# Optimization experiments

Hardware: AMD Instinct MI355X
Metric: run time of the kernel (lower is better)

## Reference

```python
import jax, jax.numpy as jnp
import numpy as np

B, C, H, W = 256, 3, 256, 256
ROT_DEG = 180.0
COLOR = 0.3
CROP = 256


def _sample_bilinear(img, ix, iy, zeros_pad):
    # img: [B,C,H,W]; ix, iy: [B,Ho,Wo] pixel-space coords
    Hh, Ww = img.shape[2], img.shape[3]
    x0 = jnp.floor(ix)
    y0 = jnp.floor(iy)
    wx = ix - x0
    wy = iy - y0

    def gather(yy, xx):
        yc = jnp.clip(yy, 0, Hh - 1).astype(jnp.int32)
        xc = jnp.clip(xx, 0, Ww - 1).astype(jnp.int32)
        v = jax.vmap(lambda im, y, x: im[:, y, x])(img, yc, xc)  # [B,C,Ho,Wo]
        if zeros_pad:  # torch grid_sample padding_mode='zeros': zero each OOB corner
            valid = ((yy >= 0) & (yy <= Hh - 1) & (xx >= 0) & (xx <= Ww - 1))
            v = v * valid[:, None].astype(img.dtype)
        return v

    return (gather(y0, x0) * ((1 - wy) * (1 - wx))[:, None]
            + gather(y0, x0 + 1) * ((1 - wy) * wx)[:, None]
            + gather(y0 + 1, x0) * (wy * (1 - wx))[:, None]
            + gather(y0 + 1, x0 + 1) * (wy * wx)[:, None])


def setup_inputs() -> dict:
    key = jax.random.key(0)
    ks = jax.random.split(key, 8)
    return {
        'images': jax.random.normal(ks[0], (B, C, H, W), dtype=jnp.float32),
        'rand_theta': jax.random.uniform(ks[1], (B,), dtype=jnp.float32),
        'rand_flip': jax.random.uniform(ks[2], (B,), dtype=jnp.float32),
        'rand_sizes': jax.random.uniform(ks[3], (B, 2), dtype=jnp.float32),
        'rand_shifts': jax.random.uniform(ks[4], (B, 2), dtype=jnp.float32),
        'rand_delta': jax.random.uniform(ks[5], (B, 1, 1, 1), dtype=jnp.float32),
        'rand_mag1': jax.random.uniform(ks[6], (B, 1, 1, 1), dtype=jnp.float32),
        'rand_mag2': jax.random.uniform(ks[7], (B, 1, 1, 1), dtype=jnp.float32),
    }


def reference(images, rand_theta, rand_flip, rand_sizes, rand_shifts,
              rand_delta, rand_mag1, rand_mag2):
    b, c, h, w = images.shape
    dt = images.dtype

    # ---- per-sample rotation: affine_grid + grid_sample (align_corners=False, zeros pad)
    theta = (rand_theta * 2 - 1) * (ROT_DEG * np.pi / 180.0)
    cth, sth = jnp.cos(theta), jnp.sin(theta)  # G_inv = rotate2d(theta)
    xn = (2 * jnp.arange(w, dtype=dt) + 1) / w - 1  # [W] normalized coords
    yn = (2 * jnp.arange(h, dtype=dt) + 1) / h - 1  # [H]
    xg = xn[None, None, :]
    yg = yn[None, :, None]
    xp = cth[:, None, None] * xg - sth[:, None, None] * yg  # [B,H,W]
    yp = sth[:, None, None] * xg + cth[:, None, None] * yg
    ix = ((xp + 1) * w - 1) / 2
    iy = ((yp + 1) * h - 1) / 2
    images = _sample_bilinear(images, ix, iy, zeros_pad=True)

    # ---- random horizontal flip
    flip = rand_flip > 0.5
    images = jnp.where(flip[:, None, None, None], images[..., ::-1], images)

    # ---- per-sample zoom (bilinear resize, align_corners=True) + shifted center crop
    sizes = jnp.round(h * (rand_sizes / 4 + 1.0) - 0.5)  # [B,2], values in [256, 320]
    max_shifts = sizes - CROP
    shift_ranges = max_shifts - 1e-5
    shifts = jnp.round(rand_shifts * shift_ranges - shift_ranges / 2)
    start = jnp.floor(max_shifts / 2) + shifts  # crop start (sh, sw), [B,2]
    ys = jnp.arange(h, dtype=dt)
    xs = jnp.arange(w, dtype=dt)
    # crop pixel (y,x) in the resized image maps to source coord via align_corners=True
    sy = (start[:, 0:1] + ys[None, :]) * (h - 1) / (sizes[:, 0:1] - 1)  # [B,H]
    sx = (start[:, 1:2] + xs[None, :]) * (w - 1) / (sizes[:, 1:2] - 1)  # [B,W]
    sy = jnp.clip(sy, 0, h - 1)
    sx = jnp.clip(sx, 0, w - 1)
    iy2 = jnp.broadcast_to(sy[:, :, None], (b, h, w))
    ix2 = jnp.broadcast_to(sx[:, None, :], (b, h, w))
    images = _sample_bilinear(images, ix2, iy2, zeros_pad=False)

    # ---- color jitter chain
    delta = (rand_delta * 2 - 1) * COLOR
    images = images + delta
    mag1 = (rand_mag1 * 2 - 1) * COLOR + 1
    x_mean = images.mean(axis=1, keepdims=True)
    images = (images - x_mean) * mag1 + x_mean
    mag2 = (rand_mag2 * 2 - 1) * COLOR + 1
    x_mean = images.mean(axis=(1, 2, 3), keepdims=True)
    images = (images - x_mean) * mag2 + x_mean
    return images
```

## Files before the change

kernel.cpp:

```cpp
#include <hip/hip_runtime.h>
#include <math.h>

#define Bn 256
#define Cc 3
#define Hh 256
#define Ww 256
#define HW (Hh*Ww)
#define CHW (Cc*HW)

#define P_BASE 256
#define P_STRIDE 10

#define TS 16
#define RY 29
#define RXS 33
#define PLANE1 (RY*RXS)
#define N1 (Cc*PLANE1)
#define S2 18
#define S2S 20
#define PLANE2 (S2*S2S)

typedef float f4v __attribute__((ext_vector_type(4)));

__global__ void setup_params(const float* __restrict__ th, const float* __restrict__ fl,
                             const float* __restrict__ sz, const float* __restrict__ sh,
                             const float* __restrict__ de, const float* __restrict__ m1,
                             const float* __restrict__ m2, float* __restrict__ ws) {
    int b = threadIdx.x;
    ws[b] = 0.0f;
    float* p = ws + P_BASE + b * P_STRIDE;
    float theta = (th[b] * 2.0f - 1.0f) * 3.14159265358979323846f;
    p[0] = cosf(theta);
    p[1] = sinf(theta);
    p[2] = (fl[b] > 0.5f) ? 1.0f : 0.0f;
    #pragma unroll
    for (int d = 0; d < 2; d++) {
        float s     = rintf(256.0f * (sz[b*2 + d] * 0.25f + 1.0f) - 0.5f);
        float ms    = s - 256.0f;
        float sr    = ms - 1e-5f;
        float shf   = rintf(sh[b*2 + d] * sr - sr * 0.5f);
        float start = floorf(ms * 0.5f) + shf;
        p[3 + 2*d]  = start;
        p[4 + 2*d]  = 255.0f / (s - 1.0f);
    }
    p[7] = (de[b] * 2.0f - 1.0f) * 0.3f;
    p[8] = (m1[b] * 2.0f - 1.0f) * 0.3f + 1.0f;
    p[9] = (m2[b] * 2.0f - 1.0f) * 0.3f + 1.0f;
}

__global__ __launch_bounds__(256)
void tile_params(const float* __restrict__ wsp, float* __restrict__ out) {
    const int b = blockIdx.x;
    const int t = threadIdx.x;
    const int tileY = t & 0xF0;
    const int tileX = (t & 15) << 4;
    const float* p = wsp + P_BASE + b * P_STRIDE;
    const float cth = p[0], sth = p[1];
    const bool  flip = p[2] > 0.5f;
    const float startY = p[3], scaleY = p[4];
    const float startX = p[5], scaleX = p[6];
    const bool  mir = (cth * sth) < 0.0f;

    float sy0 = fminf(fmaxf((startY + (float)tileY) * scaleY, 0.0f), 255.0f);
    float sx0 = fminf(fmaxf((startX + (float)tileX) * scaleX, 0.0f), 255.0f);
    const int rYi = (int)floorf(sy0);
    const int rXi = (int)floorf(sx0);

    const int Ymax = min(rYi + S2 - 1, 255);
    const int Xt1  = min(rXi + S2 - 1, 255);
    const int Xf0  = flip ? 255 - Xt1 : rXi;
    const int Xf1  = flip ? 255 - rXi : Xt1;
    const float xg0 = fmaf((float)Xf0, 0.0078125f, -0.99609375f);
    const float xg1 = fmaf((float)Xf1, 0.0078125f, -0.99609375f);
    const float yg0 = fmaf((float)rYi, 0.0078125f, -0.99609375f);
    const float yg1 = fmaf((float)Ymax,0.0078125f, -0.99609375f);

    float ixmin = 1e30f, iymin = 1e30f, ixmax = -1e30f, iymax = -1e30f;
    #pragma unroll
    for (int cy = 0; cy < 2; cy++) {
        #pragma unroll
        for (int cx = 0; cx < 2; cx++) {
            float xg = cx ? xg1 : xg0;
            float yg = cy ? yg1 : yg0;
            float xp = cth * xg - sth * yg;
            float yp = sth * xg + cth * yg;
            float tx = fmaf(xp, 128.0f, 127.5f);
            float ty = fmaf(yp, 128.0f, 127.5f);
            ixmin = fminf(ixmin, tx); ixmax = fmaxf(ixmax, tx);
            iymin = fminf(iymin, ty); iymax = fmaxf(iymax, ty);
        }
    }
    const int bx0  = (int)floorf(ixmin) - 1;
    const int by0  = (int)floorf(iymin) - 1;
    const int bx0a = bx0 & ~3;
    const int rneed = min(RY, (int)floorf(iymax) - by0 + 3);
    const int cneed = min(32, (int)floorf(ixmax) - bx0a + 3);
    const bool interior = (ixmin >= 0.0f) && (iymin >= 0.0f) &&
                          (ixmax < 255.0f) && (iymax < 255.0f);
    const bool affineOK = (rYi <= 255 - (S2 - 1)) && (rXi <= 255 - (S2 - 1));
    const bool fastA    = (bx0a >= 0) && (bx0a <= 224);
    const int flags = (mir ? 1 : 0) | ((interior && affineOK) ? 2 : 0)
                    | (fastA ? 4 : 0);

    const int Xfs = flip ? 255 - rXi : rXi;
    float xg = fmaf((float)Xfs, 0.0078125f, -0.99609375f);
    float yg = fmaf((float)rYi, 0.0078125f, -0.99609375f);
    float xp = cth * xg - sth * yg;
    float yp = sth * xg + cth * yg;
    float ix00 = fmaf(xp, 128.0f, 127.5f);
    float iy00 = fmaf(yp, 128.0f, 127.5f);

    float* tp = out + (size_t)b * CHW + (tileY << 8) + tileX;
    tp[0] = (float)bx0a;  tp[1] = (float)by0;
    tp[2] = (float)rYi;   tp[3] = (float)rXi;
    tp[4] = (float)flags; tp[5] = ix00; tp[6] = iy00;
    tp[7] = (float)rneed; tp[8] = (float)cneed;
}

#define PHASE_B_GENERAL(MIR)                                                  \
    for (int i = tid; i < S2 * S2; i += 256) {                                \
        int lY = i / S2;                                                      \
        int lX = i - lY * S2;                                                 \
        int Yc = min(rY + lY, 255);                                           \
        int Xc = min(rX + lX, 255);                                           \
        int Xf = flip ? 255 - Xc : Xc;                                        \
        float xg = fmaf((float)Xf, 0.0078125f, -0.99609375f);                 \
        float yg = fmaf((float)Yc, 0.0078125f, -0.99609375f);                 \
        float xp = cth * xg - sth * yg;                                       \
        float yp = sth * xg + cth * yg;                                       \
        float ixf = fmaf(xp, 128.0f, 127.5f);                                 \
        float iyf = fmaf(yp, 128.0f, 127.5f);                                 \
        float x0f = floorf(ixf), y0f = floorf(iyf);                           \
        float fx = ixf - x0f, fy = iyf - y0f;                                 \
        float wx0 = (x0f >=  0.0f && x0f <= 255.0f) ? (1.0f - fx) : 0.0f;     \
        float wx1 = (x0f >= -1.0f && x0f <= 254.0f) ? fx          : 0.0f;     \
        float wy0 = (y0f >=  0.0f && y0f <= 255.0f) ? (1.0f - fy) : 0.0f;     \
        float wy1 = (y0f >= -1.0f && y0f <= 254.0f) ? fy          : 0.0f;     \
        int ax = (int)x0f - bx0a;                                             \
        int ay = (int)y0f - by0;                                              \
        int base = ay * RXS + (MIR ? (30 - ax) : ax);                         \
        float A0 = MIR ? wx1 : wx0;                 \
        float A1 = MIR ? wx0 : wx1;                                           \
        float w00 = wy0 * A0, w01 = wy0 * A1;                                 \
        float w10 = wy1 * A0, w11 = wy1 * A1;                                 \
        int ob = lY * S2S + lX;                                               \
        _Pragma("unroll")                                                     \
        for (int c = 0; c < Cc; c++) {                                        \
            const float* Lc = L1 + c * PLANE1;                                \
            float v = w00 * Lc[base]       + w01 * Lc[base + 1]               \
                    + w10 * Lc[base + RXS] + w11 * Lc[base + RXS + 1];        \
            L2[c * PLANE2 + ob] = v;                                          \
        }                                                                     \
    }

#define B_SITE_AFFINE(MIR, LYv, LXv)                                          \
    {                                                                         \
        float lXf = (float)(LXv), lYf = (float)(LYv);                         \
        float ixf = fmaf(lYf, DxY, fmaf(lXf, DxX, ix00));                     \
        float iyf = fmaf(lYf, DyY, fmaf(lXf, DyX, iy00));                     \
        float x0f = floorf(ixf), y0f = floorf(iyf);                           \
        float fx = ixf - x0f, fy = iyf - y0f;                                 \
        int ax = (int)x0f - bx0a;                                             \
        int ay = (int)y0f - by0;                                              \
        int base = ay * RXS + (MIR ? (30 - ax) : ax);                         \
        float A0 = MIR ? fx : (1.0f - fx);                                    \
        float A1 = MIR ? (1.0f - fx) : fx;                                    \
        float wy0 = 1.0f - fy;                                                \
        float w00 = wy0 * A0, w01 = wy0 * A1;                                 \
        float w10 = fy * A0,  w11 = fy * A1;                                  \
        int ob = (LYv) * S2S + (LXv);                                         \
        _Pragma("unroll")                                                     \
        for (int c = 0; c < Cc; c++) {                                        \
            const float* Lc = L1 + c * PLANE1;                                \
            float v = w00 * Lc[base]       + w01 * Lc[base + 1]               \
                    + w10 * Lc[base + RXS] + w11 * Lc[base + RXS + 1];        \
            L2[c * PLANE2 + ob] = v;                                          \
        }                                                                     \
    }

#define PHASE_B_AFFINE(MIR)                                                   \
    {                                                                         \
        { int lY = tid >> 4, lX = tid & 15; B_SITE_AFFINE(MIR, lY, lX) }      \
        if (tid < 68) {                                                       \
            bool top = tid < 36;                                              \
            int j = tid - 36;                                                 \
            int lY = top ? (16 + (tid >= 18 ? 1 : 0)) : (j >> 1);             \
            int lX = top ? (tid - (tid >= 18 ? 18 : 0)) : (16 + (j & 1));     \
            B_SITE_AFFINE(MIR, lY, lX)                                        \
        }                                                                     \
    }

__global__ __launch_bounds__(256)
void augment_main(const float* __restrict__ img, const float* __restrict__ wsp,
                  float* out, float* __restrict__ sums) {
    __shared__ float L1[N1];
    __shared__ float L2[Cc*PLANE2];
    __shared__ float wred[4];

    const int tid = threadIdx.x;

    const int lin = blockIdx.x + (blockIdx.y << 4) + (blockIdx.z << 8);
    const int nid = (lin & 7) * (65536 / 8) + (lin >> 3);
    const int b     = nid >> 8;
    const int tileY = ((nid >> 4) & 15) << 4;
    const int tileX = (nid & 15) << 4;

    const float* p = wsp + P_BASE + b * P_STRIDE;
    const float cth = p[0], sth = p[1];
    const bool  flip = p[2] > 0.5f;
    const float startY = p[3], scaleY = p[4];
    const float startX = p[5], scaleX = p[6];
    const float delta = p[7], mag1 = p[8];

    const float* tp = out + (size_t)b * CHW + (tileY << 8) + tileX;
    const int   bx0a = (int)tp[0], by0 = (int)tp[1];
    const int   rY   = (int)tp[2], rX  = (int)tp[3];
    const int   flags = (int)tp[4];
    const float ix00 = tp[5], iy00 = tp[6];
    const int   rneed = (int)tp[7], cneed = (int)tp[8];
    const bool mir   = (flags & 1) != 0;
    const bool v0    = (flags & 2) != 0;
    const bool fastA = (flags & 4) != 0;

    const float DxX = flip ? -cth : cth;
    const float DyX = flip ? -sth : sth;
    const float DxY = -sth;
    const float DyY = cth;

    const float* imgb = img + (size_t)b * CHW;
    {
        const int r  = tid >> 3;
        const int c4 = (tid & 7) << 2;
        if (r < rneed && c4 < cneed) {
            const int ry = min(max(by0 + r, 0), 255);
            const float* srow = imgb + (ry << 8);
            if (fastA) {
                const float* s0 = srow + bx0a + c4;
                if (!mir) {
                    float* d = L1 + r * RXS + c4;
                    #pragma unroll
                    for (int ch = 0; ch < Cc; ch++) {
                        float4 v = *(const float4*)(s0 + (ch << 16));
                        float* dd = d + ch * PLANE1;
                        dd[0] = v.x; dd[1] = v.y; dd[2] = v.z; dd[3] = v.w;
                    }
                } else {
                    float* d = L1 + r * RXS + (28 - c4);
                    #pragma unroll
                    for (int ch = 0; ch < Cc; ch++) {
                        float4 v = *(const float4*)(s0 + (ch << 16));
                        float* dd = d + ch * PLANE1;
                        dd[0] = v.w; dd[1] = v.z; dd[2] = v.y; dd[3] = v.x;
                    }
                }
            } else {
                #pragma unroll
                for (int j = 0; j < 4; j++) {
                    int gx = min(max(bx0a + c4 + j, 0), 255);
                    int sx = mir ? (31 - (c4 + j)) : (c4 + j);
                    #pragma unroll
                    for (int ch = 0; ch < Cc; ch++)
                        L1[ch * PLANE1 + r * RXS + sx] = srow[(ch << 16) + gx];
                }
            }
        }
    }
    __syncthreads();

    if (v0) {
        if (mir) { PHASE_B_AFFINE(true) } else { PHASE_B_AFFINE(false) }
    } else {
        if (mir) { PHASE_B_GENERAL(true) } else { PHASE_B_GENERAL(false) }
    }
    __syncthreads();

    const int py = tid >> 4, px = tid & 15;
    const int y = tileY + py, x = tileX + px;
    float sy = fminf(fmaxf((startY + (float)y) * scaleY, 0.0f), 255.0f);
    float sx = fminf(fmaxf((startX + (float)x) * scaleX, 0.0f), 255.0f);
    float y0f = floorf(sy), x0f = floorf(sx);
    float fy = sy - y0f, fx = sx - x0f;
    int ly = (int)y0f - rY;
    int lx = (int)x0f - rX;
    int ib2 = ly * S2S + lx;
    float w00 = (1.0f - fy) * (1.0f - fx), w01 = (1.0f - fy) * fx;
    float w10 = fy * (1.0f - fx),          w11 = fy * fx;

    float vv[3];
    #pragma unroll
    for (int c = 0; c < Cc; c++) {
        const float* Lc = L2 + c * PLANE2;
        vv[c] = w00 * Lc[ib2]       + w01 * Lc[ib2 + 1]
              + w10 * Lc[ib2 + S2S] + w11 * Lc[ib2 + S2S + 1];
    }
    float mc  = (vv[0] + vv[1] + vv[2]) * (1.0f/3.0f);
    float mck = fmaf(-mag1, mc, mc) + delta;
    float s5 = 0.0f;
    float* outb = out + (size_t)b * CHW + (y << 8) + x;
    #pragma unroll
    for (int c = 0; c < Cc; c++) {
        float v5 = fmaf(vv[c], mag1, mck);
        outb[c * HW] = v5;
        s5 += v5;
    }
    #pragma unroll
    for (int off = 32; off > 0; off >>= 1) s5 += __shfl_down(s5, off, 64);
    int lane = tid & 63, wid = tid >> 6;
    if (lane == 0) wred[wid] = s5;
    __syncthreads();
    if (tid == 0) atomicAdd(&sums[b], wred[0] + wred[1] + wred[2] + wred[3]);
}

__global__ __launch_bounds__(256)
void finalize_k(float* __restrict__ out, const float* __restrict__ wsp) {
    const int b = blockIdx.y;
    const float m    = wsp[b] * (1.0f / (float)CHW);
    const float mag2 = wsp[P_BASE + b * P_STRIDE + 9];
    f4v* ob = (f4v*)(out + (size_t)b * CHW);
    const int i0 = blockIdx.x * 256 + threadIdx.x;
    #pragma unroll
    for (int k = 0; k < 12; k++) {
        int idx = i0 + k * 4096;
        f4v v = __builtin_nontemporal_load(&ob[idx]);
        v.x = fmaf(v.x - m, mag2, m);
        v.y = fmaf(v.y - m, mag2, m);
        v.z = fmaf(v.z - m, mag2, m);
        v.w = fmaf(v.w - m, mag2, m);
        __builtin_nontemporal_store(v, &ob[idx]);
    }
}

extern "C" void kernel_launch(void* const* d_in, const int* in_sizes, int n_in,
                              void* d_out, int out_size, void* d_ws, size_t ws_size,
                              hipStream_t stream) {
    const float* img = (const float*)d_in[0];
    const float* th  = (const float*)d_in[1];
    const float* fl  = (const float*)d_in[2];
    const float* sz  = (const float*)d_in[3];
    const float* sh  = (const float*)d_in[4];
    const float* de  = (const float*)d_in[5];
    const float* m1  = (const float*)d_in[6];
    const float* m2  = (const float*)d_in[7];
    float* out = (float*)d_out;
    float* ws  = (float*)d_ws;

    hipLaunchKernelGGL(setup_params, dim3(1), dim3(256), 0, stream,
                       th, fl, sz, sh, de, m1, m2, ws);
    hipLaunchKernelGGL(tile_params, dim3(Bn), dim3(256), 0, stream,
                       ws, out);
    hipLaunchKernelGGL(augment_main, dim3(Ww/TS, Hh/TS, Bn), dim3(256), 0, stream,
                       img, ws, out, ws);
    hipLaunchKernelGGL(finalize_k, dim3(16, Bn), dim3(256), 0, stream,
                       out, ws);
}
```

Before: 452.6 us.

## Fuse tile parameter computation into main kernel and pack channel pairs in LDS

Removes the separate tile_params launch that wrote per-tile parameters into the output buffer. Each block of the main kernel now recomputes those values redundantly from the per-sample params instead of reading them back. The intermediate LDS plane is split into a float2 array for channels 0-1 and a float array for channel 2, so loads can be vectorized. Bilinear interpolation is rewritten in lerp form, and per-row and per-column resize parameters are precomputed into small shared tables. The cost is a little redundant scalar math per block and a changed LDS layout that may affect bank conflicts.

```diff
diff --git a/kernel.cpp b/kernel.cpp
--- a/kernel.cpp
+++ b/kernel.cpp
@@ -20,6 +20,7 @@
 #define S2S 20
 #define PLANE2 (S2*S2S)
 
+typedef float f2v __attribute__((ext_vector_type(2)));
 typedef float f4v __attribute__((ext_vector_type(4)));
 
 __global__ void setup_params(const float* __restrict__ th, const float* __restrict__ fl,
@@ -46,75 +47,6 @@
     p[7] = (de[b] * 2.0f - 1.0f) * 0.3f;
     p[8] = (m1[b] * 2.0f - 1.0f) * 0.3f + 1.0f;
     p[9] = (m2[b] * 2.0f - 1.0f) * 0.3f + 1.0f;
-}
-
-__global__ __launch_bounds__(256)
-void tile_params(const float* __restrict__ wsp, float* __restrict__ out) {
-    const int b = blockIdx.x;
-    const int t = threadIdx.x;
-    const int tileY = t & 0xF0;
-    const int tileX = (t & 15) << 4;
-    const float* p = wsp + P_BASE + b * P_STRIDE;
-    const float cth = p[0], sth = p[1];
-    const bool  flip = p[2] > 0.5f;
-    const float startY = p[3], scaleY = p[4];
-    const float startX = p[5], scaleX = p[6];
-    const bool  mir = (cth * sth) < 0.0f;
-
-    float sy0 = fminf(fmaxf((startY + (float)tileY) * scaleY, 0.0f), 255.0f);
-    float sx0 = fminf(fmaxf((startX + (float)tileX) * scaleX, 0.0f), 255.0f);
-    const int rYi = (int)floorf(sy0);
-    const int rXi = (int)floorf(sx0);
-
-    const int Ymax = min(rYi + S2 - 1, 255);
-    const int Xt1  = min(rXi + S2 - 1, 255);
-    const int Xf0  = flip ? 255 - Xt1 : rXi;
-    const int Xf1  = flip ? 255 - rXi : Xt1;
-    const float xg0 = fmaf((float)Xf0, 0.0078125f, -0.99609375f);
-    const float xg1 = fmaf((float)Xf1, 0.0078125f, -0.99609375f);
-    const float yg0 = fmaf((float)rYi, 0.0078125f, -0.99609375f);
-    const float yg1 = fmaf((float)Ymax,0.0078125f, -0.99609375f);
-
-    float ixmin = 1e30f, iymin = 1e30f, ixmax = -1e30f, iymax = -1e30f;
-    #pragma unroll
-    for (int cy = 0; cy < 2; cy++) {
-        #pragma unroll
-        for (int cx = 0; cx < 2; cx++) {
-            float xg = cx ? xg1 : xg0;
-            float yg = cy ? yg1 : yg0;
-            float xp = cth * xg - sth * yg;
-            float yp = sth * xg + cth * yg;
-            float tx = fmaf(xp, 128.0f, 127.5f);
-            float ty = fmaf(yp, 128.0f, 127.5f);
-            ixmin = fminf(ixmin, tx); ixmax = fmaxf(ixmax, tx);
-            iymin = fminf(iymin, ty); iymax = fmaxf(iymax, ty);
-        }
-    }
-    const int bx0  = (int)floorf(ixmin) - 1;
-    const int by0  = (int)floorf(iymin) - 1;
-    const int bx0a = bx0 & ~3;
-    const int rneed = min(RY, (int)floorf(iymax) - by0 + 3);
-    const int cneed = min(32, (int)floorf(ixmax) - bx0a + 3);
-    const bool interior = (ixmin >= 0.0f) && (iymin >= 0.0f) &&
-                          (ixmax < 255.0f) && (iymax < 255.0f);
-    const bool affineOK = (rYi <= 255 - (S2 - 1)) && (rXi <= 255 - (S2 - 1));
-    const bool fastA    = (bx0a >= 0) && (bx0a <= 224);
-    const int flags = (mir ? 1 : 0) | ((interior && affineOK) ? 2 : 0)
-                    | (fastA ? 4 : 0);
-
-    const int Xfs = flip ? 255 - rXi : rXi;
-    float xg = fmaf((float)Xfs, 0.0078125f, -0.99609375f);
-    float yg = fmaf((float)rYi, 0.0078125f, -0.99609375f);
-    float xp = cth * xg - sth * yg;
-    float yp = sth * xg + cth * yg;
-    float ix00 = fmaf(xp, 128.0f, 127.5f);
-    float iy00 = fmaf(yp, 128.0f, 127.5f);
-
-    float* tp = out + (size_t)b * CHW + (tileY << 8) + tileX;
-    tp[0] = (float)bx0a;  tp[1] = (float)by0;
-    tp[2] = (float)rYi;   tp[3] = (float)rXi;
-    tp[4] = (float)flags; tp[5] = ix00; tp[6] = iy00;
-    tp[7] = (float)rneed; tp[8] = (float)cneed;
 }
 
 #define PHASE_B_GENERAL(MIR)                                                  \
@@ -144,13 +76,15 @@
         float w00 = wy0 * A0, w01 = wy0 * A1;                                 \
         float w10 = wy1 * A0, w11 = wy1 * A1;                                 \
         int ob = lY * S2S + lX;                                               \
+        float vch[3];                                                         \
         _Pragma("unroll")                                                     \
         for (int c = 0; c < Cc; c++) {                                        \
             const float* Lc = L1 + c * PLANE1;                                \
-            float v = w00 * Lc[base]       + w01 * Lc[base + 1]               \
-                    + w10 * Lc[base + RXS] + w11 * Lc[base + RXS + 1];        \
-            L2[c * PLANE2 + ob] = v;                                          \
+            vch[c] = w00 * Lc[base]       + w01 * Lc[base + 1]                \
+                   + w10 * Lc[base + RXS] + w11 * Lc[base + RXS + 1];         \
         }                                                                     \
+        L2a[ob] = (f2v){vch[0], vch[1]};                                      \
+        L2b[ob] = vch[2];                                                     \
     }
 
 #define B_SITE_AFFINE(MIR, LYv, LXv)                                          \
@@ -159,23 +93,28 @@
         float ixf = fmaf(lYf, DxY, fmaf(lXf, DxX, ix00));                     \
         float iyf = fmaf(lYf, DyY, fmaf(lXf, DyX, iy00));                     \
         float x0f = floorf(ixf), y0f = floorf(iyf);                           \
-        float fx = ixf - x0f, fy = iyf - y0f;                                 \
+        float fxe = ixf - x0f;                                                \
+        if (MIR) fxe = 1.0f - fxe;                                            \
+        float fy = iyf - y0f;                                                 \
         int ax = (int)x0f - bx0a;                                             \
         int ay = (int)y0f - by0;                                              \
         int base = ay * RXS + (MIR ? (30 - ax) : ax);                         \
-        float A0 = MIR ? fx : (1.0f - fx);                                    \
-        float A1 = MIR ? (1.0f - fx) : fx;                                    \
-        float wy0 = 1.0f - fy;                                                \
-        float w00 = wy0 * A0, w01 = wy0 * A1;                                 \
-        float w10 = fy * A0,  w11 = fy * A1;                                  \
+        const float* Lb = L1 + base;                                          \
+        f2v A  = {Lb[0],          Lb[PLANE1]};                                \
+        f2v Bt = {Lb[1],          Lb[PLANE1+1]};                              \
+        f2v Ct = {Lb[RXS],        Lb[PLANE1+RXS]};                            \
+        f2v Dt = {Lb[RXS+1],      Lb[PLANE1+RXS+1]};                          \
+        float a2 = Lb[2*PLANE1],     b2 = Lb[2*PLANE1+1];                     \
+        float c2 = Lb[2*PLANE1+RXS], d2 = Lb[2*PLANE1+RXS+1];                 \
+        f2v t0 = A  + fxe * (Bt - A);                                         \
+        f2v t1 = Ct + fxe * (Dt - Ct);                                        \
+        f2v v01 = t0 + fy * (t1 - t0);                                        \
+        float u0 = fmaf(fxe, b2 - a2, a2);                                    \
+        float u1 = fmaf(fxe, d2 - c2, c2);                                    \
+        float v2s = fmaf(fy, u1 - u0, u0);                                    \
         int ob = (LYv) * S2S + (LXv);                                         \
-        _Pragma("unroll")                                                     \
-        for (int c = 0; c < Cc; c++) {                                        \
-            const float* Lc = L1 + c * PLANE1;                                \
-            float v = w00 * Lc[base]       + w01 * Lc[base + 1]               \
-                    + w10 * Lc[base + RXS] + w11 * Lc[base + RXS + 1];        \
-            L2[c * PLANE2 + ob] = v;                                          \
-        }                                                                     \
+        L2a[ob] = v01;                                                        \
+        L2b[ob] = v2s;                                                        \
     }
 
 #define PHASE_B_AFFINE(MIR)                                                   \
@@ -192,9 +131,12 @@
 
 __global__ __launch_bounds__(256)
 void augment_main(const float* __restrict__ img, const float* __restrict__ wsp,
-                  float* out, float* __restrict__ sums) {
+                  float* __restrict__ out, float* __restrict__ sums) {
     __shared__ float L1[N1];
-    __shared__ float L2[Cc*PLANE2];
+    __shared__ f2v   L2a[PLANE2];
+    __shared__ float L2b[PLANE2];
+    __shared__ f2v   rowPar[16];
+    __shared__ f2v   colPar[16];
     __shared__ float wred[4];
 
     const int tid = threadIdx.x;
@@ -211,21 +153,77 @@
     const float startY = p[3], scaleY = p[4];
     const float startX = p[5], scaleX = p[6];
     const float delta = p[7], mag1 = p[8];
-
-    const float* tp = out + (size_t)b * CHW + (tileY << 8) + tileX;
-    const int   bx0a = (int)tp[0], by0 = (int)tp[1];
-    const int   rY   = (int)tp[2], rX  = (int)tp[3];
-    const int   flags = (int)tp[4];
-    const float ix00 = tp[5], iy00 = tp[6];
-    const int   rneed = (int)tp[7], cneed = (int)tp[8];
-    const bool mir   = (flags & 1) != 0;
-    const bool v0    = (flags & 2) != 0;
-    const bool fastA = (flags & 4) != 0;
+    const bool  mir = (cth * sth) < 0.0f;
+
+    float sy0 = fminf(fmaxf((startY + (float)tileY) * scaleY, 0.0f), 255.0f);
+    float sx0 = fminf(fmaxf((startX + (float)tileX) * scaleX, 0.0f), 255.0f);
+    const float rYf = floorf(sy0), rXf = floorf(sx0);
+    const int rY = (int)rYf;
+    const int rX = (int)rXf;
+
+    const int Ymax = min(rY + S2 - 1, 255);
+    const int Xt1  = min(rX + S2 - 1, 255);
+    const int Xf0  = flip ? 255 - Xt1 : rX;
+    const int Xf1  = flip ? 255 - rX  : Xt1;
+    const float xg0 = fmaf((float)Xf0, 0.0078125f, -0.99609375f);
+    const float xg1 = fmaf((float)Xf1, 0.0078125f, -0.99609375f);
+    const float yg0 = fmaf((float)rY,  0.0078125f, -0.99609375f);
+    const float yg1 = fmaf((float)Ymax,0.0078125f, -0.99609375f);
+
+    float ixmin = 1e30f, iymin = 1e30f, ixmax = -1e30f, iymax = -1e30f;
+    #pragma unroll
+    for (int cy = 0; cy < 2; cy++) {
+        #pragma unroll
+        for (int cx = 0; cx < 2; cx++) {
+            float xg = cx ? xg1 : xg0;
+            float yg = cy ? yg1 : yg0;
+            float xp = cth * xg - sth * yg;
+            float yp = sth * xg + cth * yg;
+            float tx = fmaf(xp, 128.0f, 127.5f);
+            float ty = fmaf(yp, 128.0f, 127.5f);
+            ixmin = fminf(ixmin, tx); ixmax = fmaxf(ixmax, tx);
+            iymin = fminf(iymin, ty); iymax = fmaxf(iymax, ty);
+        }
+    }
+    float ix00, iy00;
+    {
+        const int Xfs = flip ? 255 - rX : rX;
+        float xgs = fmaf((float)Xfs, 0.0078125f, -0.99609375f);
+        float xps = cth * xgs - sth * yg0;
+        float yps = sth * xgs + cth * yg0;
+        ix00 = fmaf(xps, 128.0f, 127.5f);
+        iy00 = fmaf(yps, 128.0f, 127.5f);
+    }
+    const int bx0  = (int)floorf(ixmin) - 1;
+    const int by0  = (int)floorf(iymin) - 1;
+    const int bx0a = bx0 & ~3;
+    const int rneed = min(RY, (int)floorf(iymax) - by0 + 3);
+    const int cneed = min(32, (int)floorf(ixmax) - bx0a + 3);
+    const bool interior = (ixmin >= 0.0f) && (iymin >= 0.0f) &&
+                          (ixmax < 255.0f) && (iymax < 255.0f);
+    const bool affineOK = (rY <= 255 - (S2 - 1)) && (rX <= 255 - (S2 - 1));
+    const bool v0    = interior && affineOK;
+    const bool fastA = (bx0a >= 0) && (bx0a <= 224);
 
     const float DxX = flip ? -cth : cth;
     const float DyX = flip ? -sth : sth;
     const float DxY = -sth;
     const float DyY = cth;
+
+    if (tid < 32) {
+        const int i = tid & 15;
+        const bool isRow = tid < 16;
+        float start = isRow ? startY : startX;
+        float scale = isRow ? scaleY : scaleX;
+        float rf    = isRow ? rYf : rXf;
+        float gf    = (float)((isRow ? tileY : tileX) + i);
+        float s  = fminf(fmaxf((start + gf) * scale, 0.0f), 255.0f);
+        float s0 = floorf(s);
+        f2v pr;
+        pr.x = (s0 - rf) * (isRow ? (float)S2S : 1.0f);
+        pr.y = s - s0;
+        (isRow ? rowPar : colPar)[i] = pr;
+    }
 
     const float* imgb = img + (size_t)b * CHW;
     {
@@ -276,23 +274,23 @@
 
     const int py = tid >> 4, px = tid & 15;
     const int y = tileY + py, x = tileX + px;
-    float sy = fminf(fmaxf((startY + (float)y) * scaleY, 0.0f), 255.0f);
-    float sx = fminf(fmaxf((startX + (float)x) * scaleX, 0.0f), 255.0f);
-    float y0f = floorf(sy), x0f = floorf(sx);
-    float fy = sy - y0f, fx = sx - x0f;
-    int ly = (int)y0f - rY;
-    int lx = (int)x0f - rX;
-    int ib2 = ly * S2S + lx;
-    float w00 = (1.0f - fy) * (1.0f - fx), w01 = (1.0f - fy) * fx;
-    float w10 = fy * (1.0f - fx),          w11 = fy * fx;
-
-    float vv[3];
-    #pragma unroll
-    for (int c = 0; c < Cc; c++) {
-        const float* Lc = L2 + c * PLANE2;
-        vv[c] = w00 * Lc[ib2]       + w01 * Lc[ib2 + 1]
-              + w10 * Lc[ib2 + S2S] + w11 * Lc[ib2 + S2S + 1];
-    }
+    f2v rp = rowPar[py];
+    f2v cp = colPar[px];
+    const int ib2 = (int)(rp.x + cp.x);
+    const float fy = rp.y, fx = cp.y;
+
+    f2v Av = L2a[ib2],       Bv = L2a[ib2 + 1];
+    f2v Cv = L2a[ib2 + S2S], Dv = L2a[ib2 + S2S + 1];
+    f2v t0 = Av + fx * (Bv - Av);
+    f2v t1 = Cv + fx * (Dv - Cv);
+    f2v v01 = t0 + fy * (t1 - t0);
+    float a2 = L2b[ib2],       b2 = L2b[ib2 + 1];
+    float c2 = L2b[ib2 + S2S], d2 = L2b[ib2 + S2S + 1];
+    float u0 = fmaf(fx, b2 - a2, a2);
+    float u1 = fmaf(fx, d2 - c2, c2);
+    float v2s = fmaf(fy, u1 - u0, u0);
+
+    float vv[3] = {v01.x, v01.y, v2s};
     float mc  = (vv[0] + vv[1] + vv[2]) * (1.0f/3.0f);
     float mck = fmaf(-mag1, mc, mc) + delta;
     float s5 = 0.0f;
@@ -346,8 +344,6 @@
 
     hipLaunchKernelGGL(setup_params, dim3(1), dim3(256), 0, stream,
                        th, fl, sz, sh, de, m1, m2, ws);
-    hipLaunchKernelGGL(tile_params, dim3(Bn), dim3(256), 0, stream,
-                       ws, out);
     hipLaunchKernelGGL(augment_main, dim3(Ww/TS, Hh/TS, Bn), dim3(256), 0, stream,
                        img, ws, out, ws);
     hipLaunchKernelGGL(finalize_k, dim3(16, Bn), dim3(256), 0, stream,
```

Result: no change. 453.8 us (+0.3%).
